# Kernel optimization log

Measured on AMD Instinct MI355X. Metric: run time of the kernel, lower is better.

## Reference

```python
import jax, jax.numpy as jnp
import numpy as np

T, B, D, H, GH = 512, 512, 512, 512, 32  # time, batch, input_dim, hidden_dim, gate-MLP hidden


def setup_inputs() -> dict:
    key = jax.random.key(0)
    ks = jax.random.split(key, 5)
    inputs = jax.random.normal(ks[0], (T, B, D), jnp.float32)
    hx = jnp.zeros((B, H), jnp.float32)
    cx = jnp.zeros((B, H), jnp.float32)
    in1 = D + H
    s1 = 1.0 / np.sqrt(in1)
    s2 = 1.0 / np.sqrt(GH)
    # 4 gates stacked on leading axis: order = (forget, input, update, output)
    W1 = jax.random.uniform(ks[1], (4, in1, GH), jnp.float32, -s1, s1)
    b1 = jax.random.uniform(ks[2], (4, GH), jnp.float32, -s1, s1)
    W2 = jax.random.uniform(ks[3], (4, GH, H), jnp.float32, -s2, s2)
    b2 = jax.random.uniform(ks[4], (4, H), jnp.float32, -s2, s2)
    return dict(inputs=inputs, hx=hx, cx=cx, W1=W1, b1=b1, W2=W2, b2=b2)


def reference(inputs, hx, cx, W1, b1, W2, b2):
    def step(carry, x):
        h, c = carry
        comb = jnp.concatenate([x, h], axis=1)  # [B, D+H]
        z1 = jax.nn.relu(jnp.einsum('bi,gij->gbj', comb, W1) + b1[:, None, :])  # [4,B,GH]
        gates = jnp.einsum('gbj,gjh->gbh', z1, W2) + b2[:, None, :]             # [4,B,H]
        f = jax.nn.sigmoid(gates[0])
        i = jax.nn.sigmoid(gates[1])
        g = jnp.tanh(gates[2])
        o = jax.nn.sigmoid(gates[3])
        c_new = f * c + i * g
        h_new = o * jnp.tanh(c_new)
        return (h_new, c_new), h_new

    (hf, cf), outputs = jax.lax.scan(step, (hx, cx), inputs)  # outputs: [T,B,H]
    return outputs, hf, cf
```

## Files before the change

kernel.cpp:

```cpp
#include <hip/hip_runtime.h>

#define T_STEPS 512
#define OUT_HFOFF ((size_t)134217728)
#define OUT_CFOFF (OUT_HFOFF + (size_t)262144)

typedef short s8v  __attribute__((ext_vector_type(8)));
typedef float f32x4 __attribute__((ext_vector_type(4)));

static __device__ __forceinline__ unsigned short f2bf(float f){
  unsigned int x = __float_as_uint(f);
  x += 0x7fffu + ((x >> 16) & 1u);
  return (unsigned short)(x >> 16);
}
static __device__ __forceinline__ float bf2f(unsigned short u){
  return __uint_as_float(((unsigned int)u) << 16);
}
static __device__ __forceinline__ float sigmoidf_(float x){
  return 1.f / (1.f + __expf(-x));
}
static __device__ __forceinline__ float tanhf_(float x){
  float e = __expf(2.f * x);
  return 1.f - 2.f / (e + 1.f);
}

__global__ void prep_kernel(const float* __restrict__ W1, const float* __restrict__ W2,
                            unsigned short* __restrict__ wxhi, unsigned short* __restrict__ wxlo,
                            unsigned short* __restrict__ w1h, unsigned short* __restrict__ w2f)
{
  unsigned u = blockIdx.x * 256u + threadIdx.x;
  {
    unsigned e = u & 7u, c = (u >> 3) & 127u, kg = (u >> 10) & 3u, kk = u >> 12;
    unsigned k = 32u*kk + 8u*kg + e;
    unsigned g = c >> 5, j = c & 31u;
    float v = W1[((size_t)g*1024u + k)*32u + j];
    unsigned short hi = f2bf(v);
    wxhi[u] = hi;
    wxlo[u] = f2bf(v - bf2f(hi));
    w1h[u]  = f2bf(W1[((size_t)g*1024u + 512u + k)*32u + j]);
  }
  {
    unsigned e = u & 7u, kg = (u >> 3) & 3u, hc = (u >> 5) & 511u, g = u >> 14;
    w2f[u] = f2bf(W2[((size_t)g*32u + 8u*kg + e)*512u + hc]);
  }
}

__global__ __launch_bounds__(256, 2) void xproj_kernel(
    const float* __restrict__ x, const unsigned short* __restrict__ wxhi,
    const unsigned short* __restrict__ wxlo, const float* __restrict__ b1,
    float* __restrict__ out)
{
  __shared__ unsigned short Ahi[128*40];
  __shared__ unsigned short Alo[128*40];
  const int tid = threadIdx.x;
  const int lane = tid & 63, wv = tid >> 6;
  const int l15 = lane & 15, lg = lane >> 4;
  const int wm = wv >> 1, wn = wv & 1;
  const int m0 = blockIdx.x * 128;
  const int tstep = m0 >> 9;
  const int brow0 = m0 & 511;

  f32x4 acc[4][4];
  #pragma unroll
  for (int i = 0; i < 4; ++i)
    #pragma unroll
    for (int j = 0; j < 4; ++j){ acc[i][j][0]=0.f; acc[i][j][1]=0.f; acc[i][j][2]=0.f; acc[i][j][3]=0.f; }

  float b1v[4];
  #pragma unroll
  for (int nt = 0; nt < 4; ++nt) b1v[nt] = b1[64*wn + 16*nt + l15];

  const int srow = tid >> 1;
  const int sk   = (tid & 1) * 16;

  for (int kk = 0; kk < 16; ++kk){
    __syncthreads();
    const float* src = x + (size_t)(m0 + srow)*512 + kk*32 + sk;
    float fv[16];
    #pragma unroll
    for (int i = 0; i < 4; ++i){
      float4 v = *(const float4*)(src + 4*i);
      fv[4*i+0]=v.x; fv[4*i+1]=v.y; fv[4*i+2]=v.z; fv[4*i+3]=v.w;
    }
    #pragma unroll
    for (int i = 0; i < 8; ++i){
      float a0 = fv[2*i], a1 = fv[2*i+1];
      unsigned short h0 = f2bf(a0), h1 = f2bf(a1);
      unsigned short q0 = f2bf(a0 - bf2f(h0)), q1 = f2bf(a1 - bf2f(h1));
      *(unsigned int*)&Ahi[srow*40 + sk + 2*i] = (unsigned)h0 | ((unsigned)h1 << 16);
      *(unsigned int*)&Alo[srow*40 + sk + 2*i] = (unsigned)q0 | ((unsigned)q1 << 16);
    }
    __syncthreads();

    s8v ah[4], al[4], bh[4], bl[4];
    #pragma unroll
    for (int mt = 0; mt < 4; ++mt){
      int off = (64*wm + 16*mt + l15)*40 + 8*lg;
      ah[mt] = *(const s8v*)&Ahi[off];
      al[mt] = *(const s8v*)&Alo[off];
    }
    #pragma unroll
    for (int nt = 0; nt < 4; ++nt){
      size_t idx = ((size_t)(kk*4 + lg)*128 + (64*wn + 16*nt + l15)) * 8;
      bh[nt] = *(const s8v*)&wxhi[idx];
      bl[nt] = *(const s8v*)&wxlo[idx];
    }
    #pragma unroll
    for (int mt = 0; mt < 4; ++mt)
      #pragma unroll
      for (int nt = 0; nt < 4; ++nt){
        acc[mt][nt] = __builtin_amdgcn_mfma_f32_16x16x32_bf16(ah[mt], bh[nt], acc[mt][nt], 0,0,0);
        acc[mt][nt] = __builtin_amdgcn_mfma_f32_16x16x32_bf16(ah[mt], bl[nt], acc[mt][nt], 0,0,0);
        acc[mt][nt] = __builtin_amdgcn_mfma_f32_16x16x32_bf16(al[mt], bh[nt], acc[mt][nt], 0,0,0);
      }
  }

  #pragma unroll
  for (int mt = 0; mt < 4; ++mt)
    #pragma unroll
    for (int nt = 0; nt < 4; ++nt){
      int c = 64*wn + 16*nt + l15;
      #pragma unroll
      for (int r = 0; r < 4; ++r){
        int b = brow0 + 64*wm + 16*mt + 4*lg + r;
        size_t o = ((size_t)(tstep*512 + (b & ~1)))*512 + (size_t)(b & 1)*128 + c;
        out[o] = acc[mt][nt][r] + b1v[nt];
      }
    }
}

__global__ __launch_bounds__(256, 1) void rec_kernel(
    const float* __restrict__ hx, const float* __restrict__ cx,
    const float* __restrict__ b2, const unsigned short* __restrict__ w1hf,
    const unsigned short* __restrict__ w2f, float* __restrict__ out)
{
  __shared__ unsigned short hbuf[64*144];
  __shared__ unsigned short z1buf[16*144];
  __shared__ float gatesS[8*512];

  const int tid = threadIdx.x;
  const int lane = tid & 63, wv = tid >> 6;
  const int l15 = lane & 15, lg = lane >> 4;
  const int b0 = blockIdx.x * 2;
  const int col2 = tid * 2;

  s8v w1h[16][2];
  #pragma unroll
  for (int kk = 0; kk < 16; ++kk)
    #pragma unroll
    for (int nt = 0; nt < 2; ++nt){
      size_t idx = ((size_t)(kk*4 + lg)*128 + (32*wv + 16*nt + l15)) * 8;
      w1h[kk][nt] = *(const s8v*)&w1hf[idx];
    }
  s8v w2r[4][8];
  #pragma unroll
  for (int g = 0; g < 4; ++g)
    #pragma unroll
    for (int nt = 0; nt < 8; ++nt){
      size_t idx = ((size_t)(g*512 + (128*wv + 16*nt + l15))*4 + lg) * 8;
      w2r[g][nt] = *(const s8v*)&w2f[idx];
    }

  float creg[2][2], hreg[2][2], b2r[4][2];
  #pragma unroll
  for (int r = 0; r < 2; ++r){
    creg[r][0] = cx[(size_t)(b0+r)*512 + col2];
    creg[r][1] = cx[(size_t)(b0+r)*512 + col2 + 1];
    hreg[r][0] = 0.f; hreg[r][1] = 0.f;
  }
  #pragma unroll
  for (int g = 0; g < 4; ++g){
    b2r[g][0] = b2[(size_t)g*512 + col2];
    b2r[g][1] = b2[(size_t)g*512 + col2 + 1];
  }

  for (int i = tid; i < 64*144; i += 256) hbuf[i] = 0;
  __syncthreads();
  {
    const int kk = col2 >> 5, kg = (col2 >> 3) & 3, e = col2 & 7;
    char* base = (char*)hbuf + (kk*4 + kg)*288 + e*2;
    #pragma unroll
    for (int r = 0; r < 2; ++r){
      float h0v = hx[(size_t)(b0+r)*512 + col2];
      float h1v = hx[(size_t)(b0+r)*512 + col2 + 1];
      *(unsigned int*)(base + r*16) = (unsigned)f2bf(h0v) | ((unsigned)f2bf(h1v) << 16);
    }
  }
  __syncthreads();

  float xp[2][2] = {{0.f,0.f},{0.f,0.f}};
  if (lg == 0){
    const float* xb = out + ((size_t)b0)*512;
    #pragma unroll
    for (int nt = 0; nt < 2; ++nt)
      #pragma unroll
      for (int r = 0; r < 2; ++r)
        xp[nt][r] = xb[r*128 + 32*wv + 16*nt + l15];
  }

  for (int ts = 0; ts < T_STEPS; ++ts){
    float xpn[2][2] = {{0.f,0.f},{0.f,0.f}};
    if (lg == 0 && ts + 1 < T_STEPS){
      const float* xb = out + ((size_t)((ts+1)*512 + b0))*512;
      #pragma unroll
      for (int nt = 0; nt < 2; ++nt)
        #pragma unroll
        for (int r = 0; r < 2; ++r)
          xpn[nt][r] = xb[r*128 + 32*wv + 16*nt + l15];
    }

    f32x4 acc0; acc0[0]=0.f; acc0[1]=0.f; acc0[2]=0.f; acc0[3]=0.f;
    f32x4 acc1 = acc0;
    #pragma unroll
    for (int kk = 0; kk < 16; ++kk){
      s8v af = *(const s8v*)((char*)hbuf + (kk*4 + lg)*288 + l15*16);
      acc0 = __builtin_amdgcn_mfma_f32_16x16x32_bf16(af, w1h[kk][0], acc0, 0,0,0);
      acc1 = __builtin_amdgcn_mfma_f32_16x16x32_bf16(af, w1h[kk][1], acc1, 0,0,0);
    }
    #pragma unroll
    for (int nt = 0; nt < 2; ++nt){
      f32x4 a = nt ? acc1 : acc0;
      int cz = 32*wv + 16*nt + l15;
      int g = cz >> 5, j = cz & 31;
      char* zb = (char*)z1buf + (g*4 + (j>>3))*288 + (j&7)*2;
      #pragma unroll
      for (int rr = 0; rr < 4; ++rr){
        float v = a[rr];
        if (lg == 0 && rr < 2) v += xp[nt][rr];
        v = fmaxf(v, 0.f);
        *(unsigned short*)(zb + (4*lg + rr)*16) = f2bf(v);
      }
    }
    __syncthreads();

    s8v zf[4];
    #pragma unroll
    for (int g = 0; g < 4; ++g)
      zf[g] = *(const s8v*)((char*)z1buf + (g*4 + lg)*288 + l15*16);
    f32x4 z4; z4[0]=0.f; z4[1]=0.f; z4[2]=0.f; z4[3]=0.f;
    #pragma unroll
    for (int nt = 0; nt < 8; ++nt){
      f32x4 ga[4];
      #pragma unroll
      for (int g = 0; g < 4; ++g)
        ga[g] = __builtin_amdgcn_mfma_f32_16x16x32_bf16(zf[g], w2r[g][nt], z4, 0,0,0);
      if (lg == 0){
        int c = 128*wv + 16*nt + l15;
        #pragma unroll
        for (int g = 0; g < 4; ++g){
          gatesS[(g*2 + 0)*512 + c] = ga[g][0];
          gatesS[(g*2 + 1)*512 + c] = ga[g][1];
        }
      }
    }

    #pragma unroll
    for (int r = 0; r < 2; ++r){
      #pragma unroll
      for (int i = 0; i < 2; ++i){
        int c = col2 + i;
        float F = sigmoidf_(gatesS[(0*2 + r)*512 + c] + b2r[0][i]);
        float I = sigmoidf_(gatesS[(1*2 + r)*512 + c] + b2r[1][i]);
        float G = tanhf_  (gatesS[(2*2 + r)*512 + c] + b2r[2][i]);
        float O = sigmoidf_(gatesS[(3*2 + r)*512 + c] + b2r[3][i]);
        float cn = F*creg[r][i] + I*G;
        float hn = O*tanhf_(cn);
        creg[r][i] = cn; hreg[r][i] = hn;
      }
      float2 st; st.x = hreg[r][0]; st.y = hreg[r][1];
      *(float2*)(out + ((size_t)(ts*512 + b0 + r))*512 + col2) = st;
      const int kk = col2 >> 5, kg = (col2 >> 3) & 3, e = col2 & 7;
      *(unsigned int*)((char*)hbuf + (kk*4 + kg)*288 + r*16 + e*2) =
          (unsigned)f2bf(hreg[r][0]) | ((unsigned)f2bf(hreg[r][1]) << 16);
    }
    __syncthreads();

    #pragma unroll
    for (int nt = 0; nt < 2; ++nt)
      #pragma unroll
      for (int r = 0; r < 2; ++r)
        xp[nt][r] = xpn[nt][r];
  }

  #pragma unroll
  for (int r = 0; r < 2; ++r){
    float2 hv; hv.x = hreg[r][0]; hv.y = hreg[r][1];
    *(float2*)(out + OUT_HFOFF + (size_t)(b0+r)*512 + col2) = hv;
    float2 cv; cv.x = creg[r][0]; cv.y = creg[r][1];
    *(float2*)(out + OUT_CFOFF + (size_t)(b0+r)*512 + col2) = cv;
  }
}

extern "C" void kernel_launch(void* const* d_in, const int* in_sizes, int n_in,
                              void* d_out, int out_size, void* d_ws, size_t ws_size,
                              hipStream_t stream)
{
  const float* x   = (const float*)d_in[0];
  const float* hx  = (const float*)d_in[1];
  const float* cx  = (const float*)d_in[2];
  const float* W1  = (const float*)d_in[3];
  const float* b1  = (const float*)d_in[4];
  const float* W2  = (const float*)d_in[5];
  const float* b2  = (const float*)d_in[6];
  float* out = (float*)d_out;

  unsigned short* wsb  = (unsigned short*)d_ws;
  unsigned short* wxhi = wsb;
  unsigned short* wxlo = wsb + 65536;
  unsigned short* w1h  = wsb + 131072;
  unsigned short* w2f  = wsb + 196608;

  prep_kernel <<<256, 256, 0, stream>>>(W1, W2, wxhi, wxlo, w1h, w2f);
  xproj_kernel<<<2048, 256, 0, stream>>>(x, wxhi, wxlo, b1, out);
  rec_kernel  <<<256, 256, 0, stream>>>(hx, cx, b2, w1h, w2f, out);
}
```

Before: 2.134 ms.

## Stage x-projection and h outputs in LDS, split MFMA accumulator chains

Each block now loads the precomputed input projection for 16 timesteps at a time into LDS and reads it from there every step. Hidden-state outputs are buffered in LDS and flushed to global memory once every 16 steps, instead of a per-step global load and store sitting on the serial recurrence path. The h·W1 MFMA chain is split into four independent accumulators that are summed at the end, which shortens the dependency chain between MFMAs. Gate reads from LDS are also widened to float2. The cost is about 80KB of extra LDS and a burst of global traffic every 16 steps.

```diff
diff --git a/kernel.cpp b/kernel.cpp
--- a/kernel.cpp
+++ b/kernel.cpp
@@ -136,6 +136,8 @@
   __shared__ unsigned short hbuf[64*144];
   __shared__ unsigned short z1buf[16*144];
   __shared__ float gatesS[8*512];
+  __shared__ float xpLDS[16*256];
+  __shared__ float houtLDS[16*1024];
 
   const int tid = threadIdx.x;
   const int lane = tid & 63, wv = tid >> 6;
@@ -185,37 +187,44 @@
       *(unsigned int*)(base + r*16) = (unsigned)f2bf(h0v) | ((unsigned)f2bf(h1v) << 16);
     }
   }
+
+  {
+    #pragma unroll
+    for (int i = 0; i < 4; ++i){
+      int flat = i*1024 + tid*4;
+      int s = flat >> 8, off = flat & 255;
+      float4 v = *(const float4*)(out + ((size_t)(s*512 + b0))*512 + off);
+      *(float4*)&xpLDS[flat] = v;
+    }
+  }
   __syncthreads();
 
-  float xp[2][2] = {{0.f,0.f},{0.f,0.f}};
-  if (lg == 0){
-    const float* xb = out + ((size_t)b0)*512;
-    #pragma unroll
-    for (int nt = 0; nt < 2; ++nt)
-      #pragma unroll
-      for (int r = 0; r < 2; ++r)
-        xp[nt][r] = xb[r*128 + 32*wv + 16*nt + l15];
-  }
-
   for (int ts = 0; ts < T_STEPS; ++ts){
-    float xpn[2][2] = {{0.f,0.f},{0.f,0.f}};
-    if (lg == 0 && ts + 1 < T_STEPS){
-      const float* xb = out + ((size_t)((ts+1)*512 + b0))*512;
+    f32x4 p0[4], p1[4];
+    #pragma unroll
+    for (int t = 0; t < 4; ++t){
+      p0[t][0]=0.f; p0[t][1]=0.f; p0[t][2]=0.f; p0[t][3]=0.f;
+      p1[t][0]=0.f; p1[t][1]=0.f; p1[t][2]=0.f; p1[t][3]=0.f;
+    }
+    #pragma unroll
+    for (int kk = 0; kk < 16; ++kk){
+      s8v af = *(const s8v*)((char*)hbuf + (kk*4 + lg)*288 + l15*16);
+      p0[kk>>2] = __builtin_amdgcn_mfma_f32_16x16x32_bf16(af, w1h[kk][0], p0[kk>>2], 0,0,0);
+      p1[kk>>2] = __builtin_amdgcn_mfma_f32_16x16x32_bf16(af, w1h[kk][1], p1[kk>>2], 0,0,0);
+    }
+    f32x4 acc0 = (p0[0] + p0[1]) + (p0[2] + p0[3]);
+    f32x4 acc1 = (p1[0] + p1[1]) + (p1[2] + p1[3]);
+
+    float xpv[2][2];
+    if (lg == 0){
+      const int xb = (ts & 15) * 256;
       #pragma unroll
       for (int nt = 0; nt < 2; ++nt)
         #pragma unroll
         for (int r = 0; r < 2; ++r)
-          xpn[nt][r] = xb[r*128 + 32*wv + 16*nt + l15];
-    }
-
-    f32x4 acc0; acc0[0]=0.f; acc0[1]=0.f; acc0[2]=0.f; acc0[3]=0.f;
-    f32x4 acc1 = acc0;
-    #pragma unroll
-    for (int kk = 0; kk < 16; ++kk){
-      s8v af = *(const s8v*)((char*)hbuf + (kk*4 + lg)*288 + l15*16);
-      acc0 = __builtin_amdgcn_mfma_f32_16x16x32_bf16(af, w1h[kk][0], acc0, 0,0,0);
-      acc1 = __builtin_amdgcn_mfma_f32_16x16x32_bf16(af, w1h[kk][1], acc1, 0,0,0);
-    }
+          xpv[nt][r] = xpLDS[xb + r*128 + 32*wv + 16*nt + l15];
+    }
+
     #pragma unroll
     for (int nt = 0; nt < 2; ++nt){
       f32x4 a = nt ? acc1 : acc0;
@@ -225,7 +234,7 @@
       #pragma unroll
       for (int rr = 0; rr < 4; ++rr){
         float v = a[rr];
-        if (lg == 0 && rr < 2) v += xp[nt][rr];
+        if (lg == 0 && rr < 2) v += xpv[nt][rr];
         v = fmaxf(v, 0.f);
         *(unsigned short*)(zb + (4*lg + rr)*16) = f2bf(v);
       }
@@ -257,28 +266,47 @@
     for (int r = 0; r < 2; ++r){
       #pragma unroll
       for (int i = 0; i < 2; ++i){
-        int c = col2 + i;
-        float F = sigmoidf_(gatesS[(0*2 + r)*512 + c] + b2r[0][i]);
-        float I = sigmoidf_(gatesS[(1*2 + r)*512 + c] + b2r[1][i]);
-        float G = tanhf_  (gatesS[(2*2 + r)*512 + c] + b2r[2][i]);
-        float O = sigmoidf_(gatesS[(3*2 + r)*512 + c] + b2r[3][i]);
+        float2 gF = *(const float2*)&gatesS[(0*2 + r)*512 + col2];
+        float2 gI = *(const float2*)&gatesS[(1*2 + r)*512 + col2];
+        float2 gG = *(const float2*)&gatesS[(2*2 + r)*512 + col2];
+        float2 gO = *(const float2*)&gatesS[(3*2 + r)*512 + col2];
+        float F = sigmoidf_((i ? gF.y : gF.x) + b2r[0][i]);
+        float I = sigmoidf_((i ? gI.y : gI.x) + b2r[1][i]);
+        float G = tanhf_  ((i ? gG.y : gG.x) + b2r[2][i]);
+        float O = sigmoidf_((i ? gO.y : gO.x) + b2r[3][i]);
         float cn = F*creg[r][i] + I*G;
         float hn = O*tanhf_(cn);
         creg[r][i] = cn; hreg[r][i] = hn;
       }
       float2 st; st.x = hreg[r][0]; st.y = hreg[r][1];
-      *(float2*)(out + ((size_t)(ts*512 + b0 + r))*512 + col2) = st;
+      *(float2*)&houtLDS[(ts & 15)*1024 + r*512 + col2] = st;
       const int kk = col2 >> 5, kg = (col2 >> 3) & 3, e = col2 & 7;
       *(unsigned int*)((char*)hbuf + (kk*4 + kg)*288 + r*16 + e*2) =
           (unsigned)f2bf(hreg[r][0]) | ((unsigned)f2bf(hreg[r][1]) << 16);
     }
+
+    if ((ts & 15) == 15 && ts + 1 < T_STEPS){
+      const int ts0n = ts + 1;
+      #pragma unroll
+      for (int i = 0; i < 4; ++i){
+        int flat = i*1024 + tid*4;
+        int s = flat >> 8, off = flat & 255;
+        float4 v = *(const float4*)(out + ((size_t)((ts0n + s)*512 + b0))*512 + off);
+        *(float4*)&xpLDS[flat] = v;
+      }
+    }
     __syncthreads();
 
-    #pragma unroll
-    for (int nt = 0; nt < 2; ++nt)
-      #pragma unroll
-      for (int r = 0; r < 2; ++r)
-        xp[nt][r] = xpn[nt][r];
+    if ((ts & 15) == 15){
+      const int ts0 = ts - 15;
+      #pragma unroll
+      for (int i = 0; i < 16; ++i){
+        int flat = i*1024 + tid*4;
+        int s = flat >> 10, r = (flat >> 9) & 1, c = flat & 511;
+        float4 v = *(const float4*)&houtLDS[flat];
+        *(float4*)(out + ((size_t)((ts0 + s)*512 + b0 + r))*512 + c) = v;
+      }
+    }
   }
 
   #pragma unroll
```

Measured after the change: 2.255 ms. +5.7%, slower.
